# Kernel tuning notes

Hardware: AMD Instinct MI355X
Metric: run time of the kernel (lower is better)

Reference implementation:

```python
import jax, jax.numpy as jnp
import numpy as np

N_NODES = 100000
N_EDGES = 1250000
D_FEAT = 64


def setup_inputs() -> dict:
    key = jax.random.key(0)
    kx, ke = jax.random.split(key)
    x = jax.random.normal(kx, (N_NODES, D_FEAT), dtype=jnp.float32)
    edge_index = jax.random.randint(ke, (2, N_EDGES), 0, N_NODES, dtype=jnp.int64)
    return {"x": x, "edge_index": edge_index}


def reference(x, edge_index):
    # propagate: scatter_nested gathers x[idxj] grouped by destination idxi
    # (a ragged per-node neighbor set); the module's sum_nested reduces each
    # group. Expressed densely and jit-ably as gather + segment-sum.
    idxi = edge_index[0, :]  # destination nodes
    idxj = edge_index[1, :]  # source nodes
    messages = x[idxj]  # [E, D] edge-level gather (memory-bound)
    out = jax.ops.segment_sum(messages, idxi, num_segments=N_NODES)  # [N, D]
    return out
```

## Files before the change

### kernel.cpp

```cpp
#include <hip/hip_runtime.h>
#include <hip/hip_fp16.h>

#define N_NODES 100000
#define N_EDGES 1250000
#define D_FEAT  64

#define NPB     392
#define NBINS   256
#define BCAP    6144
#define HALF    196
#define HCAP    3328
#define K23B    (NBINS * 2)
#define EPB     5120
#define EPT     10
#define K1B     ((N_EDGES + EPB - 1) / EPB)
#define CONVB   256
#define OVF_CAP 32768
#define XH_INTS (N_NODES * (D_FEAT / 2))

__global__ __launch_bounds__(512) void k1_bin_conv_kernel(
        const int* __restrict__ idxi, const int* __restrict__ idxj,
        int* __restrict__ gcursor, int* __restrict__ ovfcnt,
        int* __restrict__ ovf, int* __restrict__ binbuf,
        const float* __restrict__ x, unsigned int* __restrict__ xh) {
    __shared__ int hist[NBINS];
    __shared__ int runstart[NBINS];
    __shared__ int gbase[NBINS];
    __shared__ int cur[NBINS];
    __shared__ int staged[EPB];
    __shared__ unsigned char sbin[EPB];

    if (blockIdx.x >= K1B) {
        int t0 = (blockIdx.x - K1B) * 512 + threadIdx.x;
        int stride = CONVB * 512;
        const float2* x2 = (const float2*)x;
        for (int i = t0; i < XH_INTS; i += stride) {
            float2 v = x2[i];
            __half2 h = __floats2half2_rn(v.x, v.y);
            xh[i] = *(unsigned int*)&h;
        }
        return;
    }

    int t = threadIdx.x;
    if (t < NBINS) hist[t] = 0;
    __syncthreads();

    int base = blockIdx.x * EPB;
    int n = N_EDGES - base; if (n > EPB) n = EPB;

    int d[EPT], s[EPT], bn[EPT];
#pragma unroll
    for (int j = 0; j < EPT; ++j) {
        int i = t + j * 512;
        if (i < n) { d[j] = idxi[base + i]; s[j] = idxj[base + i]; }
        else       { d[j] = -1; s[j] = 0; }
    }
#pragma unroll
    for (int j = 0; j < EPT; ++j) {
        bn[j] = (d[j] >= 0) ? (d[j] / NPB) : -1;
        if (bn[j] >= 0) atomicAdd(&hist[bn[j]], 1);
    }
    __syncthreads();

    if (t < 64) {
        int b0 = t * 4;
        int h0 = hist[b0], h1 = hist[b0 + 1], h2 = hist[b0 + 2], h3 = hist[b0 + 3];
        int s01 = h0 + h1;
        int sum = s01 + h2 + h3;
        int inc = sum;
#pragma unroll
        for (int off = 1; off < 64; off <<= 1) {
            int u = __shfl_up(inc, off, 64);
            if (t >= off) inc += u;
        }
        int ex = inc - sum;
        runstart[b0]     = ex;
        runstart[b0 + 1] = ex + h0;
        runstart[b0 + 2] = ex + s01;
        runstart[b0 + 3] = ex + s01 + h2;
    }
    __syncthreads();

    if (t < NBINS) {
        int h = hist[t];
        gbase[t] = h ? atomicAdd(&gcursor[t], h) : 0;
        cur[t] = 0;
    }
    __syncthreads();

#pragma unroll
    for (int j = 0; j < EPT; ++j) {
        if (bn[j] >= 0) {
            int idx = runstart[bn[j]] + atomicAdd(&cur[bn[j]], 1);
            staged[idx] = ((d[j] - bn[j] * NPB) << 17) | s[j];
            sbin[idx] = (unsigned char)bn[j];
        }
    }
    __syncthreads();

    for (int i = t; i < n; i += 512) {
        int b = sbin[i];
        int p = staged[i];
        int tgt = gbase[b] + (i - runstart[b]);
        if (tgt < BCAP) {
            binbuf[b * BCAP + tgt] = p;
        } else {
            int op = atomicAdd(ovfcnt, 1);
            if (op < OVF_CAP) { ovf[2 * op] = b * NPB + (p >> 17); ovf[2 * op + 1] = p & 0x1FFFF; }
        }
    }
}

__device__ __forceinline__ void cvt8(uint4 u, float4& a, float4& b) {
    __half2 h0 = *reinterpret_cast<__half2*>(&u.x);
    __half2 h1 = *reinterpret_cast<__half2*>(&u.y);
    __half2 h2 = *reinterpret_cast<__half2*>(&u.z);
    __half2 h3 = *reinterpret_cast<__half2*>(&u.w);
    float2 f0 = __half22float2(h0), f1 = __half22float2(h1);
    float2 f2 = __half22float2(h2), f3 = __half22float2(h3);
    a = make_float4(f0.x, f0.y, f1.x, f1.y);
    b = make_float4(f2.x, f2.y, f3.x, f3.y);
}

__global__ __launch_bounds__(1024, 8) void k23_fp16_kernel(
        const float* __restrict__ x, const unsigned int* __restrict__ xh,
        const int* __restrict__ gcursor, const int* __restrict__ binbuf,
        const int* __restrict__ ovfcnt, const int* __restrict__ ovf,
        float* __restrict__ out) {
    __shared__ int cnt[HALF];
    __shared__ int excl[HALF];
    __shared__ int cur[HALF];
    __shared__ int srt[HCAP];
    int blk = blockIdx.x;
    int bin = blk >> 1;
    int hi  = blk & 1;
    int lobase = hi * HALF;
    int t = threadIdx.x;
    if (t < HALF) cnt[t] = 0;
    __syncthreads();

    int n = gcursor[bin];
    if (n > BCAP) n = BCAP;
    const int* src = binbuf + (size_t)bin * BCAP;

    int p[6];
#pragma unroll
    for (int j = 0; j < 6; ++j) {
        int i = t + j * 1024;
        p[j] = (i < n) ? src[i] : -1;
    }
#pragma unroll
    for (int j = 0; j < 6; ++j) {
        if (p[j] >= 0) {
            int loc = (p[j] >> 17) - lobase;
            if ((unsigned)loc < HALF) atomicAdd(&cnt[loc], 1);
            else p[j] = -1;
        }
    }
    __syncthreads();

    if (t < 64) {
        int h[4];
        int sum = 0;
#pragma unroll
        for (int q = 0; q < 4; ++q) {
            int b = t * 4 + q;
            h[q] = (b < HALF) ? cnt[b] : 0;
            sum += h[q];
        }
        int inc = sum;
#pragma unroll
        for (int off = 1; off < 64; off <<= 1) {
            int u = __shfl_up(inc, off, 64);
            if (t >= off) inc += u;
        }
        int ex = inc - sum;
#pragma unroll
        for (int q = 0; q < 4; ++q) {
            int b = t * 4 + q;
            if (b < HALF) { excl[b] = ex; cur[b] = 0; }
            ex += h[q];
        }
    }
    __syncthreads();

#pragma unroll
    for (int j = 0; j < 6; ++j) {
        if (p[j] >= 0) {
            int loc = (p[j] >> 17) - lobase;
            int pos = excl[loc] + atomicAdd(&cur[loc], 1);
            if (pos < HCAP) srt[pos] = p[j] & 0x1FFFF;
        }
    }
    __syncthreads();

    int sg = t >> 3, c8 = t & 7;
    const uint4* xp = (const uint4*)xh;
    for (int dl = sg; dl < HALF; dl += 128) {
        int node = bin * NPB + lobase + dl;
        int k = excl[dl];
        int end = k + cnt[dl];
        if (end > HCAP) end = HCAP;
        float4 accA = make_float4(0.f, 0.f, 0.f, 0.f);
        float4 accB = make_float4(0.f, 0.f, 0.f, 0.f);
        for (; k + 4 <= end; k += 4) {
            uint4 u0 = xp[(size_t)srt[k]     * 8 + c8];
            uint4 u1 = xp[(size_t)srt[k + 1] * 8 + c8];
            uint4 u2 = xp[(size_t)srt[k + 2] * 8 + c8];
            uint4 u3 = xp[(size_t)srt[k + 3] * 8 + c8];
            float4 a0, b0, a1, b1, a2, b2, a3, b3;
            cvt8(u0, a0, b0); cvt8(u1, a1, b1); cvt8(u2, a2, b2); cvt8(u3, a3, b3);
            accA.x += (a0.x + a1.x) + (a2.x + a3.x);
            accA.y += (a0.y + a1.y) + (a2.y + a3.y);
            accA.z += (a0.z + a1.z) + (a2.z + a3.z);
            accA.w += (a0.w + a1.w) + (a2.w + a3.w);
            accB.x += (b0.x + b1.x) + (b2.x + b3.x);
            accB.y += (b0.y + b1.y) + (b2.y + b3.y);
            accB.z += (b0.z + b1.z) + (b2.z + b3.z);
            accB.w += (b0.w + b1.w) + (b2.w + b3.w);
        }
        for (; k < end; ++k) {
            uint4 u0 = xp[(size_t)srt[k] * 8 + c8];
            float4 a0, b0;
            cvt8(u0, a0, b0);
            accA.x += a0.x; accA.y += a0.y; accA.z += a0.z; accA.w += a0.w;
            accB.x += b0.x; accB.y += b0.y; accB.z += b0.z; accB.w += b0.w;
        }
        if (node < N_NODES) {
            ((float4*)out)[(size_t)node * 16 + (c8 << 1)]     = accA;
            ((float4*)out)[(size_t)node * 16 + (c8 << 1) + 1] = accB;
        }
    }

    __syncthreads();
    int novf = *ovfcnt;
    if (novf > 0) {
        __threadfence();
        if (novf > OVF_CAP) novf = OVF_CAP;
        int lo = bin * NPB + lobase;
        for (int e = t; e < novf; e += 1024) {
            int dnode = ovf[2 * e];
            if ((unsigned)(dnode - lo) < HALF && dnode < N_NODES) {
                int snode = ovf[2 * e + 1];
                const float* vsrc = x + (size_t)snode * D_FEAT;
                float* o = out + (size_t)dnode * D_FEAT;
                for (int f = 0; f < D_FEAT; ++f) atomicAdd(o + f, vsrc[f]);
            }
        }
    }
}

__global__ __launch_bounds__(1024, 8) void k23_fused_kernel(
        const float* __restrict__ x, const int* __restrict__ gcursor,
        const int* __restrict__ binbuf, const int* __restrict__ ovfcnt,
        const int* __restrict__ ovf, float* __restrict__ out) {
    __shared__ int cnt[HALF];
    __shared__ int excl[HALF];
    __shared__ int cur[HALF];
    __shared__ int srt[HCAP];
    int blk = blockIdx.x;
    int bin = blk >> 1;
    int hi  = blk & 1;
    int lobase = hi * HALF;
    int t = threadIdx.x;
    if (t < HALF) cnt[t] = 0;
    __syncthreads();

    int n = gcursor[bin];
    if (n > BCAP) n = BCAP;
    const int* src = binbuf + (size_t)bin * BCAP;

    int p[6];
#pragma unroll
    for (int j = 0; j < 6; ++j) {
        int i = t + j * 1024;
        p[j] = (i < n) ? src[i] : -1;
    }
#pragma unroll
    for (int j = 0; j < 6; ++j) {
        if (p[j] >= 0) {
            int loc = (p[j] >> 17) - lobase;
            if ((unsigned)loc < HALF) atomicAdd(&cnt[loc], 1);
            else p[j] = -1;
        }
    }
    __syncthreads();

    if (t < 64) {
        int h[4];
        int sum = 0;
#pragma unroll
        for (int q = 0; q < 4; ++q) {
            int b = t * 4 + q;
            h[q] = (b < HALF) ? cnt[b] : 0;
            sum += h[q];
        }
        int inc = sum;
#pragma unroll
        for (int off = 1; off < 64; off <<= 1) {
            int u = __shfl_up(inc, off, 64);
            if (t >= off) inc += u;
        }
        int ex = inc - sum;
#pragma unroll
        for (int q = 0; q < 4; ++q) {
            int b = t * 4 + q;
            if (b < HALF) { excl[b] = ex; cur[b] = 0; }
            ex += h[q];
        }
    }
    __syncthreads();

#pragma unroll
    for (int j = 0; j < 6; ++j) {
        if (p[j] >= 0) {
            int loc = (p[j] >> 17) - lobase;
            int pos = excl[loc] + atomicAdd(&cur[loc], 1);
            if (pos < HCAP) srt[pos] = p[j] & 0x1FFFF;
        }
    }
    __syncthreads();

    int sg = t >> 4, c4 = t & 15;
    const float4* xp = (const float4*)x;
#pragma unroll
    for (int i2 = 0; i2 < 4; ++i2) {
        int dl = sg + (i2 << 6);
        if (dl >= HALF) break;
        int node = bin * NPB + lobase + dl;
        int k = excl[dl];
        int end = k + cnt[dl];
        if (end > HCAP) end = HCAP;
        float4 acc = make_float4(0.f, 0.f, 0.f, 0.f);
        for (; k + 4 <= end; k += 4) {
            int a0 = srt[k], a1 = srt[k + 1], a2 = srt[k + 2], a3 = srt[k + 3];
            float4 v0 = xp[a0 * 16 + c4];
            float4 v1 = xp[a1 * 16 + c4];
            float4 v2 = xp[a2 * 16 + c4];
            float4 v3 = xp[a3 * 16 + c4];
            acc.x += (v0.x + v1.x) + (v2.x + v3.x);
            acc.y += (v0.y + v1.y) + (v2.y + v3.y);
            acc.z += (v0.z + v1.z) + (v2.z + v3.z);
            acc.w += (v0.w + v1.w) + (v2.w + v3.w);
        }
        for (; k < end; ++k) {
            float4 v0 = xp[srt[k] * 16 + c4];
            acc.x += v0.x; acc.y += v0.y; acc.z += v0.z; acc.w += v0.w;
        }
        if (node < N_NODES)
            ((float4*)out)[(size_t)node * 16 + c4] = acc;
    }

    __syncthreads();
    int novf = *ovfcnt;
    if (novf > 0) {
        __threadfence();
        if (novf > OVF_CAP) novf = OVF_CAP;
        int lo = bin * NPB + lobase;
        for (int e = t; e < novf; e += 1024) {
            int dnode = ovf[2 * e];
            if ((unsigned)(dnode - lo) < HALF && dnode < N_NODES) {
                int snode = ovf[2 * e + 1];
                const float* vsrc = x + (size_t)snode * D_FEAT;
                float* o = out + (size_t)dnode * D_FEAT;
                for (int f = 0; f < D_FEAT; ++f) atomicAdd(o + f, vsrc[f]);
            }
        }
    }
}


__global__ __launch_bounds__(256) void zero_f4_kernel(float* __restrict__ out, int n4) {
    int i = blockIdx.x * blockDim.x + threadIdx.x;
    if (i < n4) ((float4*)out)[i] = make_float4(0.f, 0.f, 0.f, 0.f);
}

__global__ __launch_bounds__(256) void scatter_add_kernel(const float* __restrict__ x,
                                                          const int* __restrict__ idxi,
                                                          const int* __restrict__ idxj,
                                                          float* __restrict__ out) {
    int t = blockIdx.x * blockDim.x + threadIdx.x;
    int e = t >> 4;
    if (e >= N_EDGES) return;
    int fo = (t & 15) << 2;
    int dst = idxi[e];
    int src = idxj[e];
    const float4 v = *(const float4*)(x + (size_t)src * D_FEAT + fo);
    float* o = out + (size_t)dst * D_FEAT + fo;
    atomicAdd(o + 0, v.x);
    atomicAdd(o + 1, v.y);
    atomicAdd(o + 2, v.z);
    atomicAdd(o + 3, v.w);
}

extern "C" void kernel_launch(void* const* d_in, const int* in_sizes, int n_in,
                              void* d_out, int out_size, void* d_ws, size_t ws_size,
                              hipStream_t stream) {
    const float* x  = (const float*)d_in[0];
    const int*   ei = (const int*)d_in[1];
    const int*   idxi = ei;
    const int*   idxj = ei + N_EDGES;
    float* out = (float*)d_out;

    {
        size_t need = (256 + 16 + 2 * (size_t)OVF_CAP + (size_t)XH_INTS +
                       (size_t)NBINS * BCAP) * sizeof(int);
        if (ws_size >= need) {
            int* gcursor = (int*)d_ws;
            int* ovfcnt  = gcursor + 256;
            int* ovf     = ovfcnt + 16;
            unsigned int* xh = (unsigned int*)(ovf + 2 * OVF_CAP);
            int* binbuf  = (int*)(xh + XH_INTS);

            hipMemsetAsync(gcursor, 0, (256 + 16) * sizeof(int), stream);
            k1_bin_conv_kernel<<<K1B + CONVB, 512, 0, stream>>>(
                idxi, idxj, gcursor, ovfcnt, ovf, binbuf, x, xh);
            k23_fp16_kernel<<<K23B, 1024, 0, stream>>>(x, xh, gcursor, binbuf,
                                                       ovfcnt, ovf, out);
            return;
        }
    }

    {
        size_t need = (256 + 16 + 2 * (size_t)OVF_CAP +
                       (size_t)NBINS * BCAP) * sizeof(int);
        if (ws_size >= need) {
            int* gcursor = (int*)d_ws;
            int* ovfcnt  = gcursor + 256;
            int* ovf     = ovfcnt + 16;
            int* binbuf  = ovf + 2 * OVF_CAP;

            hipMemsetAsync(gcursor, 0, (256 + 16) * sizeof(int), stream);
            k1_bin_conv_kernel<<<K1B, 512, 0, stream>>>(
                idxi, idxj, gcursor, ovfcnt, ovf, binbuf, x, (unsigned int*)0);
            k23_fused_kernel<<<K23B, 1024, 0, stream>>>(x, gcursor, binbuf,
                                                        ovfcnt, ovf, out);
            return;
        }
    }

    int n4 = (N_NODES * D_FEAT) / 4;
    zero_f4_kernel<<<(n4 + 255) / 256, 256, 0, stream>>>(out, n4);
    long long total_threads = (long long)N_EDGES * 16;
    scatter_add_kernel<<<(int)((total_threads + 255) / 256), 256, 0, stream>>>(x, idxi, idxj, out);
}
```

Before: 130.5 us.

## Fuse memset, binning, fp16 conversion and aggregation into one cooperative kernel

Replaces the memset plus two-kernel pipeline with a single cooperative launch of 512 blocks, using grid.sync between zeroing the cursors, binning edges (with the fp16 conversion of x done on the spare blocks), and the per-bin gather-sum. The aim is to remove launch gaps and kernel boundaries, and to interleave the bin-to-block mapping so work spreads evenly across the chip. In exchange, block size falls from 1024 to 512 threads in the gather phase, each thread holds 12 entries instead of 6, shared memory per block rises, and occupancy is limited by cooperative residency. If the cooperative launch fails, the code falls back to the previous two-kernel path and drops the fp32 fused fallback.

```diff
diff --git a/kernel.cpp b/kernel.cpp
--- a/kernel.cpp
+++ b/kernel.cpp
@@ -1,5 +1,8 @@
 #include <hip/hip_runtime.h>
+#include <hip/hip_cooperative_groups.h>
 #include <hip/hip_fp16.h>
+
+namespace cg = cooperative_groups;
 
 #define N_NODES 100000
 #define N_EDGES 1250000
@@ -10,13 +13,250 @@
 #define BCAP    6144
 #define HALF    196
 #define HCAP    3328
-#define K23B    (NBINS * 2)
 #define EPB     5120
 #define EPT     10
 #define K1B     ((N_EDGES + EPB - 1) / EPB)
+#define COOPB   512
 #define CONVB   256
 #define OVF_CAP 32768
 #define XH_INTS (N_NODES * (D_FEAT / 2))
+
+__device__ __forceinline__ void cvt8(uint4 u, float4& a, float4& b) {
+    __half2 h0 = *reinterpret_cast<__half2*>(&u.x);
+    __half2 h1 = *reinterpret_cast<__half2*>(&u.y);
+    __half2 h2 = *reinterpret_cast<__half2*>(&u.z);
+    __half2 h3 = *reinterpret_cast<__half2*>(&u.w);
+    float2 f0 = __half22float2(h0), f1 = __half22float2(h1);
+    float2 f2 = __half22float2(h2), f3 = __half22float2(h3);
+    a = make_float4(f0.x, f0.y, f1.x, f1.y);
+    b = make_float4(f2.x, f2.y, f3.x, f3.y);
+}
+
+__global__ __launch_bounds__(512, 4) void fused_all_kernel(
+        const int* __restrict__ idxi, const int* __restrict__ idxj,
+        int* __restrict__ gcursor, int* __restrict__ ovfcnt,
+        int* __restrict__ ovf, int* __restrict__ binbuf,
+        const float* __restrict__ x, unsigned int* __restrict__ xh,
+        float* __restrict__ out) {
+    __shared__ int hist[NBINS];
+    __shared__ int runstart[NBINS];
+    __shared__ int gbase[NBINS];
+    __shared__ int cur[NBINS];
+    __shared__ int staged[EPB];
+    __shared__ unsigned char sbin[EPB];
+    __shared__ int cnt[HALF];
+    __shared__ int excl[HALF];
+    __shared__ int curh[HALF];
+    __shared__ int srt[HCAP];
+
+    cg::grid_group grid = cg::this_grid();
+    int t = threadIdx.x;
+    int bid = blockIdx.x;
+    int gtid = bid * 512 + t;
+
+    if (gtid < NBINS + 16) gcursor[gtid] = 0;
+    __threadfence();
+    grid.sync();
+
+    if (bid < K1B) {
+        if (t < NBINS) hist[t] = 0;
+        __syncthreads();
+
+        int base = bid * EPB;
+        int n = N_EDGES - base; if (n > EPB) n = EPB;
+
+        int d[EPT], s[EPT], bn[EPT];
+#pragma unroll
+        for (int j = 0; j < EPT; ++j) {
+            int i = t + j * 512;
+            if (i < n) { d[j] = idxi[base + i]; s[j] = idxj[base + i]; }
+            else       { d[j] = -1; s[j] = 0; }
+        }
+#pragma unroll
+        for (int j = 0; j < EPT; ++j) {
+            bn[j] = (d[j] >= 0) ? (d[j] / NPB) : -1;
+            if (bn[j] >= 0) atomicAdd(&hist[bn[j]], 1);
+        }
+        __syncthreads();
+
+        if (t < 64) {
+            int b0 = t * 4;
+            int h0 = hist[b0], h1 = hist[b0 + 1], h2 = hist[b0 + 2], h3 = hist[b0 + 3];
+            int s01 = h0 + h1;
+            int sum = s01 + h2 + h3;
+            int inc = sum;
+#pragma unroll
+            for (int off = 1; off < 64; off <<= 1) {
+                int u = __shfl_up(inc, off, 64);
+                if (t >= off) inc += u;
+            }
+            int ex = inc - sum;
+            runstart[b0]     = ex;
+            runstart[b0 + 1] = ex + h0;
+            runstart[b0 + 2] = ex + s01;
+            runstart[b0 + 3] = ex + s01 + h2;
+        }
+        __syncthreads();
+
+        if (t < NBINS) {
+            int h = hist[t];
+            gbase[t] = h ? atomicAdd(&gcursor[t], h) : 0;
+            cur[t] = 0;
+        }
+        __syncthreads();
+
+#pragma unroll
+        for (int j = 0; j < EPT; ++j) {
+            if (bn[j] >= 0) {
+                int idx = runstart[bn[j]] + atomicAdd(&cur[bn[j]], 1);
+                staged[idx] = ((d[j] - bn[j] * NPB) << 17) | s[j];
+                sbin[idx] = (unsigned char)bn[j];
+            }
+        }
+        __syncthreads();
+
+        for (int i = t; i < n; i += 512) {
+            int b = sbin[i];
+            int p = staged[i];
+            int tgt = gbase[b] + (i - runstart[b]);
+            if (tgt < BCAP) {
+                binbuf[b * BCAP + tgt] = p;
+            } else {
+                int op = atomicAdd(ovfcnt, 1);
+                if (op < OVF_CAP) { ovf[2 * op] = b * NPB + (p >> 17); ovf[2 * op + 1] = p & 0x1FFFF; }
+            }
+        }
+    } else {
+        int i0 = (bid - K1B) * 512 + t;
+        int stride = (COOPB - K1B) * 512;
+        const float2* x2 = (const float2*)x;
+        for (int i = i0; i < XH_INTS; i += stride) {
+            float2 v = x2[i];
+            __half2 h = __floats2half2_rn(v.x, v.y);
+            xh[i] = *(unsigned int*)&h;
+        }
+    }
+    __threadfence();
+    grid.sync();
+
+    int L = ((bid & 7) << 6) + (bid >> 3);
+    int bin = L >> 1;
+    int lobase = (L & 1) * HALF;
+
+    if (t < HALF) cnt[t] = 0;
+    __syncthreads();
+
+    int n = gcursor[bin];
+    if (n > BCAP) n = BCAP;
+    const int* src = binbuf + (size_t)bin * BCAP;
+
+    int p[12];
+#pragma unroll
+    for (int j = 0; j < 12; ++j) {
+        int i = t + j * 512;
+        p[j] = (i < n) ? src[i] : -1;
+    }
+#pragma unroll
+    for (int j = 0; j < 12; ++j) {
+        if (p[j] >= 0) {
+            int loc = (p[j] >> 17) - lobase;
+            if ((unsigned)loc < HALF) atomicAdd(&cnt[loc], 1);
+            else p[j] = -1;
+        }
+    }
+    __syncthreads();
+
+    if (t < 64) {
+        int h[4];
+        int sum = 0;
+#pragma unroll
+        for (int q = 0; q < 4; ++q) {
+            int b = t * 4 + q;
+            h[q] = (b < HALF) ? cnt[b] : 0;
+            sum += h[q];
+        }
+        int inc = sum;
+#pragma unroll
+        for (int off = 1; off < 64; off <<= 1) {
+            int u = __shfl_up(inc, off, 64);
+            if (t >= off) inc += u;
+        }
+        int ex = inc - sum;
+#pragma unroll
+        for (int q = 0; q < 4; ++q) {
+            int b = t * 4 + q;
+            if (b < HALF) { excl[b] = ex; curh[b] = 0; }
+            ex += h[q];
+        }
+    }
+    __syncthreads();
+
+#pragma unroll
+    for (int j = 0; j < 12; ++j) {
+        if (p[j] >= 0) {
+            int loc = (p[j] >> 17) - lobase;
+            int pos = excl[loc] + atomicAdd(&curh[loc], 1);
+            if (pos < HCAP) srt[pos] = p[j] & 0x1FFFF;
+        }
+    }
+    __syncthreads();
+
+    int sg = t >> 3, c8 = t & 7;
+    const uint4* xp = (const uint4*)xh;
+    for (int dl = sg; dl < HALF; dl += 64) {
+        int node = bin * NPB + lobase + dl;
+        int k = excl[dl];
+        int end = k + cnt[dl];
+        if (end > HCAP) end = HCAP;
+        float4 accA = make_float4(0.f, 0.f, 0.f, 0.f);
+        float4 accB = make_float4(0.f, 0.f, 0.f, 0.f);
+        for (; k + 4 <= end; k += 4) {
+            uint4 u0 = xp[(size_t)srt[k]     * 8 + c8];
+            uint4 u1 = xp[(size_t)srt[k + 1] * 8 + c8];
+            uint4 u2 = xp[(size_t)srt[k + 2] * 8 + c8];
+            uint4 u3 = xp[(size_t)srt[k + 3] * 8 + c8];
+            float4 a0, b0, a1, b1, a2, b2, a3, b3;
+            cvt8(u0, a0, b0); cvt8(u1, a1, b1); cvt8(u2, a2, b2); cvt8(u3, a3, b3);
+            accA.x += (a0.x + a1.x) + (a2.x + a3.x);
+            accA.y += (a0.y + a1.y) + (a2.y + a3.y);
+            accA.z += (a0.z + a1.z) + (a2.z + a3.z);
+            accA.w += (a0.w + a1.w) + (a2.w + a3.w);
+            accB.x += (b0.x + b1.x) + (b2.x + b3.x);
+            accB.y += (b0.y + b1.y) + (b2.y + b3.y);
+            accB.z += (b0.z + b1.z) + (b2.z + b3.z);
+            accB.w += (b0.w + b1.w) + (b2.w + b3.w);
+        }
+        for (; k < end; ++k) {
+            uint4 u0 = xp[(size_t)srt[k] * 8 + c8];
+            float4 a0, b0;
+            cvt8(u0, a0, b0);
+            accA.x += a0.x; accA.y += a0.y; accA.z += a0.z; accA.w += a0.w;
+            accB.x += b0.x; accB.y += b0.y; accB.z += b0.z; accB.w += b0.w;
+        }
+        if (node < N_NODES) {
+            ((float4*)out)[(size_t)node * 16 + (c8 << 1)]     = accA;
+            ((float4*)out)[(size_t)node * 16 + (c8 << 1) + 1] = accB;
+        }
+    }
+
+    __syncthreads();
+    int novf = *ovfcnt;
+    if (novf > 0) {
+        __threadfence();
+        if (novf > OVF_CAP) novf = OVF_CAP;
+        int lo = bin * NPB + lobase;
+        for (int e = t; e < novf; e += 512) {
+            int dnode = ovf[2 * e];
+            if ((unsigned)(dnode - lo) < HALF && dnode < N_NODES) {
+                int snode = ovf[2 * e + 1];
+                const float* vsrc = x + (size_t)snode * D_FEAT;
+                float* o = out + (size_t)dnode * D_FEAT;
+                for (int f = 0; f < D_FEAT; ++f) atomicAdd(o + f, vsrc[f]);
+            }
+        }
+    }
+}
+
 
 __global__ __launch_bounds__(512) void k1_bin_conv_kernel(
         const int* __restrict__ idxi, const int* __restrict__ idxj,
@@ -112,17 +352,6 @@
     }
 }
 
-__device__ __forceinline__ void cvt8(uint4 u, float4& a, float4& b) {
-    __half2 h0 = *reinterpret_cast<__half2*>(&u.x);
-    __half2 h1 = *reinterpret_cast<__half2*>(&u.y);
-    __half2 h2 = *reinterpret_cast<__half2*>(&u.z);
-    __half2 h3 = *reinterpret_cast<__half2*>(&u.w);
-    float2 f0 = __half22float2(h0), f1 = __half22float2(h1);
-    float2 f2 = __half22float2(h2), f3 = __half22float2(h3);
-    a = make_float4(f0.x, f0.y, f1.x, f1.y);
-    b = make_float4(f2.x, f2.y, f3.x, f3.y);
-}
-
 __global__ __launch_bounds__(1024, 8) void k23_fp16_kernel(
         const float* __restrict__ x, const unsigned int* __restrict__ xh,
         const int* __restrict__ gcursor, const int* __restrict__ binbuf,
@@ -134,8 +363,7 @@
     __shared__ int srt[HCAP];
     int blk = blockIdx.x;
     int bin = blk >> 1;
-    int hi  = blk & 1;
-    int lobase = hi * HALF;
+    int lobase = (blk & 1) * HALF;
     int t = threadIdx.x;
     if (t < HALF) cnt[t] = 0;
     __syncthreads();
@@ -251,125 +479,6 @@
     }
 }
 
-__global__ __launch_bounds__(1024, 8) void k23_fused_kernel(
-        const float* __restrict__ x, const int* __restrict__ gcursor,
-        const int* __restrict__ binbuf, const int* __restrict__ ovfcnt,
-        const int* __restrict__ ovf, float* __restrict__ out) {
-    __shared__ int cnt[HALF];
-    __shared__ int excl[HALF];
-    __shared__ int cur[HALF];
-    __shared__ int srt[HCAP];
-    int blk = blockIdx.x;
-    int bin = blk >> 1;
-    int hi  = blk & 1;
-    int lobase = hi * HALF;
-    int t = threadIdx.x;
-    if (t < HALF) cnt[t] = 0;
-    __syncthreads();
-
-    int n = gcursor[bin];
-    if (n > BCAP) n = BCAP;
-    const int* src = binbuf + (size_t)bin * BCAP;
-
-    int p[6];
-#pragma unroll
-    for (int j = 0; j < 6; ++j) {
-        int i = t + j * 1024;
-        p[j] = (i < n) ? src[i] : -1;
-    }
-#pragma unroll
-    for (int j = 0; j < 6; ++j) {
-        if (p[j] >= 0) {
-            int loc = (p[j] >> 17) - lobase;
-            if ((unsigned)loc < HALF) atomicAdd(&cnt[loc], 1);
-            else p[j] = -1;
-        }
-    }
-    __syncthreads();
-
-    if (t < 64) {
-        int h[4];
-        int sum = 0;
-#pragma unroll
-        for (int q = 0; q < 4; ++q) {
-            int b = t * 4 + q;
-            h[q] = (b < HALF) ? cnt[b] : 0;
-            sum += h[q];
-        }
-        int inc = sum;
-#pragma unroll
-        for (int off = 1; off < 64; off <<= 1) {
-            int u = __shfl_up(inc, off, 64);
-            if (t >= off) inc += u;
-        }
-        int ex = inc - sum;
-#pragma unroll
-        for (int q = 0; q < 4; ++q) {
-            int b = t * 4 + q;
-            if (b < HALF) { excl[b] = ex; cur[b] = 0; }
-            ex += h[q];
-        }
-    }
-    __syncthreads();
-
-#pragma unroll
-    for (int j = 0; j < 6; ++j) {
-        if (p[j] >= 0) {
-            int loc = (p[j] >> 17) - lobase;
-            int pos = excl[loc] + atomicAdd(&cur[loc], 1);
-            if (pos < HCAP) srt[pos] = p[j] & 0x1FFFF;
-        }
-    }
-    __syncthreads();
-
-    int sg = t >> 4, c4 = t & 15;
-    const float4* xp = (const float4*)x;
-#pragma unroll
-    for (int i2 = 0; i2 < 4; ++i2) {
-        int dl = sg + (i2 << 6);
-        if (dl >= HALF) break;
-        int node = bin * NPB + lobase + dl;
-        int k = excl[dl];
-        int end = k + cnt[dl];
-        if (end > HCAP) end = HCAP;
-        float4 acc = make_float4(0.f, 0.f, 0.f, 0.f);
-        for (; k + 4 <= end; k += 4) {
-            int a0 = srt[k], a1 = srt[k + 1], a2 = srt[k + 2], a3 = srt[k + 3];
-            float4 v0 = xp[a0 * 16 + c4];
-            float4 v1 = xp[a1 * 16 + c4];
-            float4 v2 = xp[a2 * 16 + c4];
-            float4 v3 = xp[a3 * 16 + c4];
-            acc.x += (v0.x + v1.x) + (v2.x + v3.x);
-            acc.y += (v0.y + v1.y) + (v2.y + v3.y);
-            acc.z += (v0.z + v1.z) + (v2.z + v3.z);
-            acc.w += (v0.w + v1.w) + (v2.w + v3.w);
-        }
-        for (; k < end; ++k) {
-            float4 v0 = xp[srt[k] * 16 + c4];
-            acc.x += v0.x; acc.y += v0.y; acc.z += v0.z; acc.w += v0.w;
-        }
-        if (node < N_NODES)
-            ((float4*)out)[(size_t)node * 16 + c4] = acc;
-    }
-
-    __syncthreads();
-    int novf = *ovfcnt;
-    if (novf > 0) {
-        __threadfence();
-        if (novf > OVF_CAP) novf = OVF_CAP;
-        int lo = bin * NPB + lobase;
-        for (int e = t; e < novf; e += 1024) {
-            int dnode = ovf[2 * e];
-            if ((unsigned)(dnode - lo) < HALF && dnode < N_NODES) {
-                int snode = ovf[2 * e + 1];
-                const float* vsrc = x + (size_t)snode * D_FEAT;
-                float* o = out + (size_t)dnode * D_FEAT;
-                for (int f = 0; f < D_FEAT; ++f) atomicAdd(o + f, vsrc[f]);
-            }
-        }
-    }
-}
-
 
 __global__ __launch_bounds__(256) void zero_f4_kernel(float* __restrict__ out, int n4) {
     int i = blockIdx.x * blockDim.x + threadIdx.x;
@@ -403,41 +512,30 @@
     const int*   idxj = ei + N_EDGES;
     float* out = (float*)d_out;
 
-    {
-        size_t need = (256 + 16 + 2 * (size_t)OVF_CAP + (size_t)XH_INTS +
-                       (size_t)NBINS * BCAP) * sizeof(int);
-        if (ws_size >= need) {
-            int* gcursor = (int*)d_ws;
-            int* ovfcnt  = gcursor + 256;
-            int* ovf     = ovfcnt + 16;
-            unsigned int* xh = (unsigned int*)(ovf + 2 * OVF_CAP);
-            int* binbuf  = (int*)(xh + XH_INTS);
-
-            hipMemsetAsync(gcursor, 0, (256 + 16) * sizeof(int), stream);
-            k1_bin_conv_kernel<<<K1B + CONVB, 512, 0, stream>>>(
-                idxi, idxj, gcursor, ovfcnt, ovf, binbuf, x, xh);
-            k23_fp16_kernel<<<K23B, 1024, 0, stream>>>(x, xh, gcursor, binbuf,
-                                                       ovfcnt, ovf, out);
-            return;
-        }
-    }
-
-    {
-        size_t need = (256 + 16 + 2 * (size_t)OVF_CAP +
-                       (size_t)NBINS * BCAP) * sizeof(int);
-        if (ws_size >= need) {
-            int* gcursor = (int*)d_ws;
-            int* ovfcnt  = gcursor + 256;
-            int* ovf     = ovfcnt + 16;
-            int* binbuf  = ovf + 2 * OVF_CAP;
-
-            hipMemsetAsync(gcursor, 0, (256 + 16) * sizeof(int), stream);
-            k1_bin_conv_kernel<<<K1B, 512, 0, stream>>>(
-                idxi, idxj, gcursor, ovfcnt, ovf, binbuf, x, (unsigned int*)0);
-            k23_fused_kernel<<<K23B, 1024, 0, stream>>>(x, gcursor, binbuf,
-                                                        ovfcnt, ovf, out);
-            return;
-        }
+    size_t need = (256 + 16 + 2 * (size_t)OVF_CAP + (size_t)XH_INTS +
+                   (size_t)NBINS * BCAP) * sizeof(int);
+    if (ws_size >= need) {
+        int* gcursor = (int*)d_ws;
+        int* ovfcnt  = gcursor + 256;
+        int* ovf     = ovfcnt + 16;
+        unsigned int* xh = (unsigned int*)(ovf + 2 * OVF_CAP);
+        int* binbuf  = (int*)(xh + XH_INTS);
+
+        void* args[] = {(void*)&idxi, (void*)&idxj, (void*)&gcursor,
+                        (void*)&ovfcnt, (void*)&ovf, (void*)&binbuf,
+                        (void*)&x, (void*)&xh, (void*)&out};
+        hipError_t rc = hipLaunchCooperativeKernel((const void*)fused_all_kernel,
+                                                   dim3(COOPB), dim3(512),
+                                                   args, 0, stream);
+        if (rc == hipSuccess) return;
+        (void)hipGetLastError();
+
+        hipMemsetAsync(gcursor, 0, (256 + 16) * sizeof(int), stream);
+        k1_bin_conv_kernel<<<K1B + CONVB, 512, 0, stream>>>(
+            idxi, idxj, gcursor, ovfcnt, ovf, binbuf, x, xh);
+        k23_fp16_kernel<<<COOPB, 1024, 0, stream>>>(x, xh, gcursor, binbuf,
+                                                    ovfcnt, ovf, out);
+        return;
     }
 
     int n4 = (N_NODES * D_FEAT) / 4;
```

New measurement: 386.7 us. 196% more time.
